# Kernel tuning notes

Measured on AMD Instinct MI355X. Metric: run time of the kernel, lower is better.

## Reference

```python
import jax, jax.numpy as jnp
import numpy as np

B, S, D = 4, 2048, 1024
LN_EPS = 1e-5
NEG_INF = -1e9


def _layernorm(x, gamma, beta):
    mu = jnp.mean(x, axis=-1, keepdims=True)
    var = jnp.var(x, axis=-1, keepdims=True)
    return (x - mu) * jax.lax.rsqrt(var + LN_EPS) * gamma + beta


def setup_inputs() -> dict:
    key = jax.random.key(0)
    k1, k2, k3, k4 = jax.random.split(key, 4)
    context = jax.random.normal(k1, (B, S, D), dtype=jnp.float32)
    eos_mask = jnp.ones((B, S, S), dtype=jnp.int64)
    prior = jax.random.uniform(k2, (B, S, S), dtype=jnp.float32)
    bound = 1.0 / np.sqrt(D)
    Wq = jax.random.uniform(k3, (D, D), dtype=jnp.float32, minval=-bound, maxval=bound)
    Wk = jax.random.uniform(k4, (D, D), dtype=jnp.float32, minval=-bound, maxval=bound)
    gamma = jnp.ones((D,), dtype=jnp.float32)
    beta = jnp.zeros((D,), dtype=jnp.float32)
    return {"context": context, "eos_mask": eos_mask, "prior": prior,
            "Wq": Wq, "Wk": Wk, "gamma": gamma, "beta": beta}


def reference(context, eos_mask, prior, Wq, Wk, gamma, beta):
    d_model = context.shape[-1]
    seq_len = context.shape[1]
    x = _layernorm(context, gamma, beta)
    q = x @ Wq.T                                   # nn.Linear, no bias
    k = x @ Wk.T
    scores = jnp.einsum('bsd,btd->bst', q, k) / jnp.sqrt(jnp.asarray(d_model, x.dtype))

    idx = jnp.arange(seq_len)
    a_sup = idx[:, None] + 1 == idx[None, :]       # superdiagonal (torch `a`)
    c_sub = idx[:, None] - 1 == idx[None, :]       # subdiagonal  (torch `c`)
    diag = idx[:, None] == idx[None, :]            # identity     (torch `b`)
    strict_lower = idx[:, None] > idx[None, :]     # tril - eye

    # mask = eos_mask & (a + c)  (Python precedence: & binds looser than +)
    mask = (eos_mask != 0) & (a_sup | c_sub)
    scores = jnp.where(mask, scores, NEG_INF)
    neibor_attn = jax.nn.softmax(scores, axis=-1)
    neibor_attn = jnp.sqrt(neibor_attn * jnp.swapaxes(neibor_attn, -1, -2) + 1e-9)
    neibor_attn = prior + (1.0 - prior) * neibor_attn

    # t = log(neibor+1e-9).masked_fill(a==0,0) @ tril  == reverse cumsum over last axis
    logn = jnp.where(a_sup, jnp.log(neibor_attn + 1e-9), 0.0)
    t = jnp.cumsum(logn[:, :, ::-1], axis=-1)[:, :, ::-1]
    # g = exp(tril @ t), keep strictly-lower part ((tril - eye) != 0)
    g = jnp.exp(jnp.cumsum(t, axis=1))
    g = jnp.where(strict_lower, g, 0.0)

    g_attn = g + jnp.swapaxes(g, -1, -2) + jnp.where(diag, neibor_attn, 1e-9)
    return g_attn, neibor_attn
```

## Files before the change

### kernel.cpp

```cpp
#include <hip/hip_runtime.h>
#include <hip/hip_bf16.h>
#include <stdint.h>

#define SS 2048
#define DD 1024
#define RR 8192

typedef _Float16 f16;
typedef _Float16 f16x8 __attribute__((ext_vector_type(8)));
typedef _Float16 f16x4 __attribute__((ext_vector_type(4)));
typedef float    f32x4 __attribute__((ext_vector_type(4)));

__device__ __forceinline__ void gl_lds16(const f16* g, f16* l) {
  __builtin_amdgcn_global_load_lds((const __attribute__((address_space(1))) void*)g,
                                   (__attribute__((address_space(3))) void*)l,
                                   16, 0, 0);
}

__global__ __launch_bounds__(256) void k_tr(const float* __restrict__ Wq,
                                            const float* __restrict__ Wk,
                                            f16* __restrict__ Wqt,
                                            f16* __restrict__ Wkt) {
  __shared__ f16 tile[64][72];
  int bid = blockIdx.x;
  const float* src = (bid & 1) ? Wk : Wq;
  f16* dst = (bid & 1) ? Wkt : Wqt;
  int tb = bid >> 1;
  int r0 = (tb >> 4) << 6, c0 = (tb & 15) << 6;
  int t = threadIdx.x;
#pragma unroll
  for (int p = 0; p < 4; ++p) {
    int r = p * 16 + (t >> 4);
    int c = (t & 15) * 4;
    float4 v = *(const float4*)(src + (size_t)(r0 + r) * DD + c0 + c);
    tile[c + 0][r] = (f16)v.x; tile[c + 1][r] = (f16)v.y;
    tile[c + 2][r] = (f16)v.z; tile[c + 3][r] = (f16)v.w;
  }
  __syncthreads();
  int orow = t >> 2, och = (t & 3) * 16;
  f16x8 a = *(const f16x8*)&tile[orow][och];
  f16x8 b = *(const f16x8*)&tile[orow][och + 8];
  f16* o = dst + (size_t)(c0 + orow) * DD + r0 + och;
  *(f16x8*)o = a;
  *(f16x8*)(o + 8) = b;
}

__global__ __launch_bounds__(256) void k_ln(const float* __restrict__ x,
                                            const float* __restrict__ gamma,
                                            const float* __restrict__ beta,
                                            f16* __restrict__ xn) {
  int row = blockIdx.x;
  int tid = threadIdx.x;
  int lane = tid & 63, w = tid >> 6;
  const float* xr = x + (size_t)row * DD;
  float4 v = ((const float4*)xr)[tid];
  float s  = v.x + v.y + v.z + v.w;
  float ss = v.x*v.x + v.y*v.y + v.z*v.z + v.w*v.w;
#pragma unroll
  for (int off = 32; off > 0; off >>= 1) {
    s  += __shfl_down(s,  off, 64);
    ss += __shfl_down(ss, off, 64);
  }
  __shared__ float r0[4], r1[4];
  if (lane == 0) { r0[w] = s; r1[w] = ss; }
  __syncthreads();
  float tot = r0[0]+r0[1]+r0[2]+r0[3];
  float tss = r1[0]+r1[1]+r1[2]+r1[3];
  float mu  = tot * (1.0f/DD);
  float var = tss * (1.0f/DD) - mu*mu;
  float inv = rsqrtf(var + 1e-5f);
  float4 g = ((const float4*)gamma)[tid];
  float4 b = ((const float4*)beta)[tid];
  f16x4 o;
  o[0] = (f16)((v.x-mu)*inv*g.x + b.x);
  o[1] = (f16)((v.y-mu)*inv*g.y + b.y);
  o[2] = (f16)((v.z-mu)*inv*g.z + b.z);
  o[3] = (f16)((v.w-mu)*inv*g.w + b.w);
  *(f16x4*)(xn + (size_t)row*DD + tid*4) = o;
}

template<int BM, int BN, int LOG2NBN>
__global__ __launch_bounds__(256) void k_gemm_t(const f16* __restrict__ A,
                                                const f16* __restrict__ Bw,
                                                f16* __restrict__ C) {
  constexpr int K  = 1024;
  constexpr int NC = 1024;
  constexpr int MF = BM / 32;
  constexpr int NF = BN / 32;
  constexpr int IA = BM / 64;
  constexpr int IB = BN / 64;
  __shared__ f16 As[BM * 32];
  __shared__ f16 Bs[BN * 32];
  int bid = blockIdx.x;
  int bm = bid >> LOG2NBN, bn = bid & ((1 << LOG2NBN) - 1);
  int tid = threadIdx.x;
  int lane = tid & 63, w = tid >> 6;
  int wm = w >> 1, wn = w & 1;

  f32x4 acc[MF][NF] = {};

  int srow = w * 16 + (lane >> 2);
  int sch  = lane & 3;
  const f16* AgI[IA];
  const f16* BgI[IB];
  f16* lAI[IA];
  f16* lBI[IB];
#pragma unroll
  for (int i = 0; i < IA; ++i) {
    AgI[i] = A + (size_t)(bm * BM + i * 64 + srow) * K + sch * 8;
    lAI[i] = As + (i * 64 + w * 16) * 32;
  }
#pragma unroll
  for (int i = 0; i < IB; ++i) {
    BgI[i] = Bw + (size_t)(bn * BN + i * 64 + srow) * K + sch * 8;
    lBI[i] = Bs + (i * 64 + w * 16) * 32;
  }

  int rlo = lane & 15, rch = (lane >> 4) * 8;

  for (int kt = 0; kt < K; kt += 32) {
    __syncthreads();
#pragma unroll
    for (int i = 0; i < IA; ++i) gl_lds16(AgI[i] + kt, lAI[i]);
#pragma unroll
    for (int i = 0; i < IB; ++i) gl_lds16(BgI[i] + kt, lBI[i]);
    __syncthreads();
    f16x8 af[MF], bf[NF];
#pragma unroll
    for (int mi = 0; mi < MF; ++mi)
      af[mi] = *(const f16x8*)(As + (wm * (BM/2) + mi * 16 + rlo) * 32 + rch);
#pragma unroll
    for (int ni = 0; ni < NF; ++ni)
      bf[ni] = *(const f16x8*)(Bs + (wn * (BN/2) + ni * 16 + rlo) * 32 + rch);
#pragma unroll
    for (int mi = 0; mi < MF; ++mi)
#pragma unroll
      for (int ni = 0; ni < NF; ++ni)
        acc[mi][ni] = __builtin_amdgcn_mfma_f32_16x16x32_f16(af[mi], bf[ni], acc[mi][ni], 0, 0, 0);
  }
  int c0 = (lane >> 4) * 4;
#pragma unroll
  for (int mi = 0; mi < MF; ++mi)
#pragma unroll
    for (int ni = 0; ni < NF; ++ni)
#pragma unroll
      for (int r = 0; r < 4; ++r) {
        int row = bm * BM + wm * (BM/2) + mi * 16 + c0 + r;
        int col = bn * BN + wn * (BN/2) + ni * 16 + rlo;
        C[(size_t)row * NC + col] = (f16)acc[mi][ni][r];
      }
}

__global__ __launch_bounds__(256) void k_dots(const f16* __restrict__ Xn,
                                              const f16* __restrict__ Y,
                                              const int* __restrict__ eos,
                                              const float* __restrict__ prior,
                                              float* __restrict__ sup,
                                              float* __restrict__ sub,
                                              int* __restrict__ e_sup,
                                              int* __restrict__ e_sub,
                                              float* __restrict__ pr_sup) {
  int pair = blockIdx.x * 4 + (threadIdx.x >> 6);
  int lane = threadIdx.x & 63;
  int b = pair / 2047;
  int s = pair - b * 2047;
  size_t r0 = ((size_t)(b * SS + s)) * DD;
  size_t r1 = r0 + DD;
  int d0 = lane * 16;
  float da = 0.f, dc = 0.f;
#pragma unroll
  for (int h = 0; h < 2; ++h) {
    f16x8 xs  = *(const f16x8*)(Xn + r0 + d0 + h*8);
    f16x8 ys1 = *(const f16x8*)(Y  + r1 + d0 + h*8);
    f16x8 ys  = *(const f16x8*)(Y  + r0 + d0 + h*8);
    f16x8 xs1 = *(const f16x8*)(Xn + r1 + d0 + h*8);
#pragma unroll
    for (int e = 0; e < 8; ++e) {
      da += (float)xs[e] * (float)ys1[e];
      dc += (float)ys[e] * (float)xs1[e];
    }
  }
#pragma unroll
  for (int off = 32; off > 0; off >>= 1) {
    da += __shfl_down(da, off, 64);
    dc += __shfl_down(dc, off, 64);
  }
  size_t ebase = (size_t)b * SS * SS;
  int bS = b * SS;
  if (lane == 0) {
    sup[bS + s]     = da * 0.03125f;
    sub[bS + s + 1] = dc * 0.03125f;
  } else if (lane == 1) {
    e_sup[bS + s] = eos[ebase + (size_t)s * SS + s + 1];
  } else if (lane == 2) {
    e_sub[bS + s + 1] = eos[ebase + (size_t)(s + 1) * SS + s];
  } else if (lane == 3) {
    pr_sup[bS + s] = prior[ebase + (size_t)s * SS + s + 1];
  }
}

__global__ __launch_bounds__(1024) void k_scan(const float* __restrict__ sup,
                                               const float* __restrict__ sub,
                                               const int* __restrict__ e_sup,
                                               const int* __restrict__ e_sub,
                                               const float* __restrict__ pr_sup,
                                               float* __restrict__ p_sup,
                                               float* __restrict__ p_sub,
                                               double* __restrict__ P) {
  int b = blockIdx.x, t = threadIdx.x;
  int bS = b * SS;
  __shared__ float  psub_sh[SS];
  __shared__ double sc[2][1024];
  float psup_loc[2];
#pragma unroll
  for (int e = 0; e < 2; ++e) {
    int s = 2*t + e;
    bool supOK = (s < SS-1) && (e_sup[bS + s] != 0);
    bool subOK = (s >= 1)   && (e_sub[bS + s] != 0);
    float ps = 0.f, pb = 0.f;
    if (supOK && subOK) {
      float Av = sup[bS + s], Cv = sub[bS + s];
      float m  = fmaxf(Av, Cv);
      float ea = expf(Av - m), eb = expf(Cv - m);
      float iv = 1.0f / (ea + eb);
      ps = ea * iv; pb = eb * iv;
    } else if (supOK) ps = 1.f;
    else if (subOK)   pb = 1.f;
    p_sup[bS + s] = ps; p_sub[bS + s] = pb;
    psub_sh[s] = pb; psup_loc[e] = ps;
  }
  __syncthreads();
  double L0 = 0.0, L1 = 0.0;
#pragma unroll
  for (int e = 0; e < 2; ++e) {
    int s = 2*t + e;
    double Lv = 0.0;
    if (s < SS-1) {
      float pr = pr_sup[bS + s];
      float vv = sqrtf(psup_loc[e] * psub_sh[s+1] + 1e-9f);
      Lv = (double)logf(pr + (1.f - pr)*vv + 1e-9f);
    }
    if (e == 0) L0 = Lv; else L1 = Lv;
  }
  double pairv = L0 + L1;
  int pp = 0;
  sc[0][t] = pairv;
  __syncthreads();
  for (int off = 1; off < 1024; off <<= 1) {
    double v = sc[pp][t];
    if (t >= off) v += sc[pp][t - off];
    sc[1 - pp][t] = v;
    pp ^= 1;
    __syncthreads();
  }
  double incl = sc[pp][t];
  double excl = incl - pairv;
  P[bS + 2*t]     = excl + L0;
  P[bS + 2*t + 1] = excl + L0 + L1;
}

__global__ __launch_bounds__(256) void k_out(const float* __restrict__ prior,
                                             const float* __restrict__ p_sup,
                                             const float* __restrict__ p_sub,
                                             const double* __restrict__ P,
                                             float* __restrict__ g_out,
                                             float* __restrict__ n_out) {
  size_t v = (size_t)blockIdx.x * 256 + threadIdx.x;
  int j4   = (int)(v & 511);
  int rowg = (int)(v >> 9);
  int s = rowg & (SS - 1);
  int b = rowg >> 11;
  size_t base = (size_t)rowg * SS + j4 * 4;
  union F4 { float4 v4; float a[4]; };
  F4 prf; prf.v4 = *(const float4*)(prior + base);
  int bS = b * SS;
  double Ps  = P[bS + s];
  double Ps2 = (s >= 2) ? P[bS + s - 2] : 0.0;
  const float SQ9 = 3.1622776601683795e-5f;
  F4 gv, nv;
#pragma unroll
  for (int e = 0; e < 4; ++e) {
    int j = j4*4 + e;
    float pr = prf.a[e];
    float vv;
    if (j == s + 1)      vv = sqrtf(p_sup[bS+s] * p_sub[bS+s+1] + 1e-9f);
    else if (j == s - 1) vv = sqrtf(p_sub[bS+s] * p_sup[bS+s-1] + 1e-9f);
    else                 vv = SQ9;
    float na = pr + (1.f - pr) * vv;
    nv.a[e] = na;
    float g;
    if (s == j) g = na;
    else if (s > j) {
      double Pj2 = (j >= 2) ? P[bS + j - 2] : 0.0;
      g = expf((float)(Ps - Pj2)) + 1e-9f;
    } else {
      g = expf((float)(P[bS + j] - Ps2)) + 1e-9f;
    }
    gv.a[e] = g;
  }
  *(float4*)(g_out + base) = gv.v4;
  *(float4*)(n_out + base) = nv.v4;
}

extern "C" void kernel_launch(void* const* d_in, const int* in_sizes, int n_in,
                              void* d_out, int out_size, void* d_ws, size_t ws_size,
                              hipStream_t stream) {
  const float* context = (const float*)d_in[0];
  const int*   eos     = (const int*)d_in[1];
  const float* prior   = (const float*)d_in[2];
  const float* Wq      = (const float*)d_in[3];
  const float* Wk      = (const float*)d_in[4];
  const float* gamma   = (const float*)d_in[5];
  const float* beta    = (const float*)d_in[6];

  char* ws = (char*)d_ws;
  float*  sup    = (float*)(ws);
  float*  sub    = (float*)(ws + 32768);
  float*  p_sup  = (float*)(ws + 65536);
  float*  p_sub  = (float*)(ws + 98304);
  double* P      = (double*)(ws + 131072);
  int*    e_sup  = (int*)(ws + 196608);
  int*    e_sub  = (int*)(ws + 229376);
  float*  pr_sup = (float*)(ws + 262144);
  const size_t smallEnd = 294912;

  const size_t XN_BYTES = (size_t)RR * DD * 2;
  const size_t Y_BYTES  = (size_t)RR * DD * 2;
  const size_t WT_BYTES = (size_t)DD * DD * 2;
  const size_t bigNeed  = XN_BYTES + Y_BYTES + 3 * WT_BYTES;
  char* big;
  if (ws_size >= smallEnd + bigNeed) big = ws + smallEnd;
  else big = (char*)d_out + ((size_t)out_size * 4 - bigNeed);
  f16* Xn  = (f16*)big;
  f16* Y   = (f16*)(big + XN_BYTES);
  f16* Wqt = (f16*)(big + XN_BYTES + Y_BYTES);
  f16* Wkt = (f16*)(big + XN_BYTES + Y_BYTES + WT_BYTES);
  f16* Mm  = (f16*)(big + XN_BYTES + Y_BYTES + 2 * WT_BYTES);

  k_tr<<<512, 256, 0, stream>>>(Wq, Wk, Wqt, Wkt);
  k_ln<<<RR, 256, 0, stream>>>(context, gamma, beta, Xn);
  k_gemm_t<64, 64, 4><<<256, 256, 0, stream>>>(Wqt, Wkt, Mm);
  k_gemm_t<128, 128, 3><<<512, 256, 0, stream>>>(Xn, Mm, Y);
  k_dots<<<2047, 256, 0, stream>>>(Xn, Y, eos, prior, sup, sub, e_sup, e_sub, pr_sup);
  k_scan<<<4, 1024, 0, stream>>>(sup, sub, e_sup, e_sub, pr_sup, p_sup, p_sub, P);
  float* g_out = (float*)d_out;
  float* n_out = g_out + (size_t)RR * SS;
  k_out<<<16384, 256, 0, stream>>>(prior, p_sup, p_sub, P, g_out, n_out);
}
```

Baseline: 125.1 us.

## Fuse LN and weight transpose, swizzle blocks across XCDs, use wave-level scan

Layernorm and the weight transpose/cast are merged into one launch, removing a kernel launch. The GEMM and dots kernels remap block indices so neighbouring tiles land on the same XCD, which should improve L2 locality on the chiplet GPU. The scan kernel replaces a 10-step LDS Hillis-Steele scan, with a barrier per step, by wave shuffles plus a per-wave prefix. These are several unrelated small changes, and total time is likely dominated by the large output-writing kernel.

```diff
diff --git a/kernel.cpp b/kernel.cpp
--- a/kernel.cpp
+++ b/kernel.cpp
@@ -17,66 +17,67 @@
                                    16, 0, 0);
 }
 
-__global__ __launch_bounds__(256) void k_tr(const float* __restrict__ Wq,
-                                            const float* __restrict__ Wk,
-                                            f16* __restrict__ Wqt,
-                                            f16* __restrict__ Wkt) {
+__global__ __launch_bounds__(256) void k_pre(const float* __restrict__ x,
+                                             const float* __restrict__ gamma,
+                                             const float* __restrict__ beta,
+                                             f16* __restrict__ xn,
+                                             const float* __restrict__ Wq,
+                                             const float* __restrict__ Wk,
+                                             f16* __restrict__ Wqt,
+                                             f16* __restrict__ Wkt) {
   __shared__ f16 tile[64][72];
-  int bid = blockIdx.x;
-  const float* src = (bid & 1) ? Wk : Wq;
-  f16* dst = (bid & 1) ? Wkt : Wqt;
-  int tb = bid >> 1;
-  int r0 = (tb >> 4) << 6, c0 = (tb & 15) << 6;
+  int bidx = blockIdx.x;
   int t = threadIdx.x;
-#pragma unroll
-  for (int p = 0; p < 4; ++p) {
-    int r = p * 16 + (t >> 4);
-    int c = (t & 15) * 4;
-    float4 v = *(const float4*)(src + (size_t)(r0 + r) * DD + c0 + c);
-    tile[c + 0][r] = (f16)v.x; tile[c + 1][r] = (f16)v.y;
-    tile[c + 2][r] = (f16)v.z; tile[c + 3][r] = (f16)v.w;
-  }
-  __syncthreads();
-  int orow = t >> 2, och = (t & 3) * 16;
-  f16x8 a = *(const f16x8*)&tile[orow][och];
-  f16x8 b = *(const f16x8*)&tile[orow][och + 8];
-  f16* o = dst + (size_t)(c0 + orow) * DD + r0 + och;
-  *(f16x8*)o = a;
-  *(f16x8*)(o + 8) = b;
-}
-
-__global__ __launch_bounds__(256) void k_ln(const float* __restrict__ x,
-                                            const float* __restrict__ gamma,
-                                            const float* __restrict__ beta,
-                                            f16* __restrict__ xn) {
-  int row = blockIdx.x;
-  int tid = threadIdx.x;
-  int lane = tid & 63, w = tid >> 6;
-  const float* xr = x + (size_t)row * DD;
-  float4 v = ((const float4*)xr)[tid];
-  float s  = v.x + v.y + v.z + v.w;
-  float ss = v.x*v.x + v.y*v.y + v.z*v.z + v.w*v.w;
-#pragma unroll
-  for (int off = 32; off > 0; off >>= 1) {
-    s  += __shfl_down(s,  off, 64);
-    ss += __shfl_down(ss, off, 64);
-  }
-  __shared__ float r0[4], r1[4];
-  if (lane == 0) { r0[w] = s; r1[w] = ss; }
-  __syncthreads();
-  float tot = r0[0]+r0[1]+r0[2]+r0[3];
-  float tss = r1[0]+r1[1]+r1[2]+r1[3];
-  float mu  = tot * (1.0f/DD);
-  float var = tss * (1.0f/DD) - mu*mu;
-  float inv = rsqrtf(var + 1e-5f);
-  float4 g = ((const float4*)gamma)[tid];
-  float4 b = ((const float4*)beta)[tid];
-  f16x4 o;
-  o[0] = (f16)((v.x-mu)*inv*g.x + b.x);
-  o[1] = (f16)((v.y-mu)*inv*g.y + b.y);
-  o[2] = (f16)((v.z-mu)*inv*g.z + b.z);
-  o[3] = (f16)((v.w-mu)*inv*g.w + b.w);
-  *(f16x4*)(xn + (size_t)row*DD + tid*4) = o;
+  if (bidx < RR) {
+    int lane = t & 63, w = t >> 6;
+    const float* xr = x + (size_t)bidx * DD;
+    float4 v = ((const float4*)xr)[t];
+    float s  = v.x + v.y + v.z + v.w;
+    float ss = v.x*v.x + v.y*v.y + v.z*v.z + v.w*v.w;
+#pragma unroll
+    for (int off = 32; off > 0; off >>= 1) {
+      s  += __shfl_down(s,  off, 64);
+      ss += __shfl_down(ss, off, 64);
+    }
+    float* r0 = (float*)&tile[0][0];
+    float* r1 = r0 + 4;
+    if (lane == 0) { r0[w] = s; r1[w] = ss; }
+    __syncthreads();
+    float tot = r0[0]+r0[1]+r0[2]+r0[3];
+    float tss = r1[0]+r1[1]+r1[2]+r1[3];
+    float mu  = tot * (1.0f/DD);
+    float var = tss * (1.0f/DD) - mu*mu;
+    float inv = rsqrtf(var + 1e-5f);
+    float4 g = ((const float4*)gamma)[t];
+    float4 b = ((const float4*)beta)[t];
+    f16x4 o;
+    o[0] = (f16)((v.x-mu)*inv*g.x + b.x);
+    o[1] = (f16)((v.y-mu)*inv*g.y + b.y);
+    o[2] = (f16)((v.z-mu)*inv*g.z + b.z);
+    o[3] = (f16)((v.w-mu)*inv*g.w + b.w);
+    *(f16x4*)(xn + (size_t)bidx*DD + t*4) = o;
+  } else {
+    int bid = bidx - RR;
+    const float* src = (bid & 1) ? Wk : Wq;
+    f16* dst = (bid & 1) ? Wkt : Wqt;
+    int tb = bid >> 1;
+    int r0 = (tb >> 4) << 6, c0 = (tb & 15) << 6;
+#pragma unroll
+    for (int p = 0; p < 4; ++p) {
+      int r = p * 16 + (t >> 4);
+      int c = (t & 15) * 4;
+      float4 v = *(const float4*)(src + (size_t)(r0 + r) * DD + c0 + c);
+      tile[c + 0][r] = (f16)v.x; tile[c + 1][r] = (f16)v.y;
+      tile[c + 2][r] = (f16)v.z; tile[c + 3][r] = (f16)v.w;
+    }
+    __syncthreads();
+    int orow = t >> 2, och = (t & 3) * 16;
+    f16x8 a = *(const f16x8*)&tile[orow][och];
+    f16x8 b = *(const f16x8*)&tile[orow][och + 8];
+    f16* o = dst + (size_t)(c0 + orow) * DD + r0 + och;
+    *(f16x8*)o = a;
+    *(f16x8*)(o + 8) = b;
+  }
 }
 
 template<int BM, int BN, int LOG2NBN>
@@ -91,7 +92,8 @@
   constexpr int IB = BN / 64;
   __shared__ f16 As[BM * 32];
   __shared__ f16 Bs[BN * 32];
-  int bid = blockIdx.x;
+  int cpx = gridDim.x >> 3;
+  int bid = (blockIdx.x & 7) * cpx + (blockIdx.x >> 3);
   int bm = bid >> LOG2NBN, bn = bid & ((1 << LOG2NBN) - 1);
   int tid = threadIdx.x;
   int lane = tid & 63, w = tid >> 6;
@@ -160,7 +162,10 @@
                                               int* __restrict__ e_sup,
                                               int* __restrict__ e_sub,
                                               float* __restrict__ pr_sup) {
-  int pair = blockIdx.x * 4 + (threadIdx.x >> 6);
+  int q = (int)gridDim.x >> 3, r7 = (int)gridDim.x & 7;
+  int xcd = blockIdx.x & 7, idx = blockIdx.x >> 3;
+  int sb = (xcd < r7 ? xcd * (q + 1) : r7 * (q + 1) + (xcd - r7) * q) + idx;
+  int pair = sb * 4 + (threadIdx.x >> 6);
   int lane = threadIdx.x & 63;
   int b = pair / 2047;
   int s = pair - b * 2047;
@@ -208,9 +213,10 @@
                                                float* __restrict__ p_sub,
                                                double* __restrict__ P) {
   int b = blockIdx.x, t = threadIdx.x;
+  int lane = t & 63, wid = t >> 6;
   int bS = b * SS;
   __shared__ float  psub_sh[SS];
-  __shared__ double sc[2][1024];
+  __shared__ double wsum[16];
   float psup_loc[2];
 #pragma unroll
   for (int e = 0; e < 2; ++e) {
@@ -243,18 +249,17 @@
     if (e == 0) L0 = Lv; else L1 = Lv;
   }
   double pairv = L0 + L1;
-  int pp = 0;
-  sc[0][t] = pairv;
+  double v = pairv;
+#pragma unroll
+  for (int off = 1; off < 64; off <<= 1) {
+    double u = __shfl_up(v, off, 64);
+    if (lane >= off) v += u;
+  }
+  if (lane == 63) wsum[wid] = v;
   __syncthreads();
-  for (int off = 1; off < 1024; off <<= 1) {
-    double v = sc[pp][t];
-    if (t >= off) v += sc[pp][t - off];
-    sc[1 - pp][t] = v;
-    pp ^= 1;
-    __syncthreads();
-  }
-  double incl = sc[pp][t];
-  double excl = incl - pairv;
+  double base = 0.0;
+  for (int wI = 0; wI < wid; ++wI) base += wsum[wI];
+  double excl = base + v - pairv;
   P[bS + 2*t]     = excl + L0;
   P[bS + 2*t + 1] = excl + L0 + L1;
 }
@@ -337,8 +342,7 @@
   f16* Wkt = (f16*)(big + XN_BYTES + Y_BYTES + WT_BYTES);
   f16* Mm  = (f16*)(big + XN_BYTES + Y_BYTES + 2 * WT_BYTES);
 
-  k_tr<<<512, 256, 0, stream>>>(Wq, Wk, Wqt, Wkt);
-  k_ln<<<RR, 256, 0, stream>>>(context, gamma, beta, Xn);
+  k_pre<<<RR + 512, 256, 0, stream>>>(context, gamma, beta, Xn, Wq, Wk, Wqt, Wkt);
   k_gemm_t<64, 64, 4><<<256, 256, 0, stream>>>(Wqt, Wkt, Mm);
   k_gemm_t<128, 128, 3><<<512, 256, 0, stream>>>(Xn, Mm, Y);
   k_dots<<<2047, 256, 0, stream>>>(Xn, Y, eos, prior, sup, sub, e_sup, e_sub, pr_sup);
```

After: 120.4 us. 1.04x faster.
